# Kernel optimization log

Measured on AMD Instinct MI355X. Metric: run time of the kernel, lower is better.

Reference implementation:

```python
import jax, jax.numpy as jnp
import numpy as np

DEPTH = 2
TWO_PI = 6.283185307179586


def _apply_ry(state, theta, axis):
    """Apply RY(theta) on qubit at `axis` of state [N,2,2,2,2]. theta: [N] or scalar."""
    half = theta * 0.5
    a0 = jnp.take(state, 0, axis=axis)  # [N,2,2,2]
    a1 = jnp.take(state, 1, axis=axis)
    c = jnp.reshape(jnp.cos(half), (-1,) + (1,) * (a0.ndim - 1))
    s = jnp.reshape(jnp.sin(half), (-1,) + (1,) * (a0.ndim - 1))
    return jnp.stack([c * a0 - s * a1, s * a0 + c * a1], axis=axis)


def _apply_cnot(state, c_axis, t_axis):
    a0 = jnp.take(state, 0, axis=c_axis)  # control=0: unchanged
    a1 = jnp.take(state, 1, axis=c_axis)  # control=1: flip target
    t_ax = t_axis - (1 if t_axis > c_axis else 0)
    a1 = jnp.flip(a1, axis=t_ax)
    return jnp.stack([a0, a1], axis=c_axis)


def _simulate(patches, weights):
    """patches: [N,4] angles. Returns <Z_i> for i=0..3, shape [N,4]. All gates real."""
    N = patches.shape[0]
    state = jnp.zeros((N, 2, 2, 2, 2), dtype=patches.dtype)
    state = state.at[:, 0, 0, 0, 0].set(1.0)
    for w in range(4):  # data encoding
        state = _apply_ry(state, patches[:, w], axis=w + 1)
    for d in range(DEPTH):  # variational layers
        for w in range(4):
            state = _apply_ry(state, weights[d, w], axis=w + 1)
        for c, t in ((0, 1), (1, 2), (2, 3)):
            state = _apply_cnot(state, c + 1, t + 1)
    probs = state * state
    zs = []
    for w in range(4):
        p0 = jnp.take(probs, 0, axis=w + 1).sum(axis=(1, 2, 3))
        p1 = jnp.take(probs, 1, axis=w + 1).sum(axis=(1, 2, 3))
        zs.append(p0 - p1)
    return jnp.stack(zs, axis=-1)  # [N,4]


def setup_inputs() -> dict:
    key = jax.random.key(0)
    k1, k2, k3, k4 = jax.random.split(key, 4)
    B = 8192
    x = jax.random.uniform(k1, (B, 1, 28, 28), dtype=jnp.float32)
    weights = jax.random.uniform(k2, (DEPTH, 4), dtype=jnp.float32) * TWO_PI
    W = jax.random.normal(k3, (10, 4 * 14 * 14), dtype=jnp.float32) * 0.02
    b = jax.random.normal(k4, (10,), dtype=jnp.float32) * 0.02
    return {"x": x, "weights": weights, "W": W, "b": b}


def reference(x, weights, W, b):
    B = x.shape[0]
    # Extract non-overlapping 2x2 patches in row-major (i,j) order;
    # within a patch, order is [(i,j),(i,j+1),(i+1,j),(i+1,j+1)] matching x[:,:,i:i+2,j:j+2].view(B,4)
    p = x.reshape(B, 14, 2, 14, 2).transpose(0, 1, 3, 2, 4).reshape(B, 196, 4)
    feats = _simulate(p.reshape(B * 196, 4), weights).reshape(B, 196 * 4)
    logits = feats @ W.T + b
    return jax.nn.log_softmax(logits, axis=-1)
```

## Files before the change

### kernel.cpp

```cpp
#include <hip/hip_runtime.h>
#include <math.h>

#define INV2PI 0.15915494309189535f

__device__ __forceinline__ float rfl(float v) {
    return __int_as_float(__builtin_amdgcn_readfirstlane(__float_as_int(v)));
}

__global__ __launch_bounds__(256, 4) void quanv_ks_kernel(
    const float* __restrict__ x,
    const float* __restrict__ wts,
    const float* __restrict__ W,
    const float* __restrict__ bias,
    float* __restrict__ out,
    int B)
{
    __shared__ float part[4][8][40];
    __shared__ float logits[8][10];
    __shared__ float lsev[8];

    const int tid   = threadIdx.x;
    const int wave  = tid >> 6, lane = tid & 63;
    const int group = wave >> 1;
    const int half  = wave & 1;
    const int imgb  = blockIdx.x * 8 + group * 4;

    float w0r[4], cw1[4], sw1[4];
#pragma unroll
    for (int q = 0; q < 4; ++q) {
        w0r[q] = rfl(wts[q] * INV2PI);
        float r = wts[4 + q] * INV2PI;
        r -= floorf(r);
        cw1[q] = __builtin_amdgcn_cosf(r);
        sw1[q] = __builtin_amdgcn_sinf(r);
    }
    const float cc  = cw1[0]*cw1[1], cs = cw1[0]*sw1[1];
    const float sc  = sw1[0]*cw1[1], ss = sw1[0]*sw1[1];
    const float ccc = cc*cw1[2], ccs = cc*sw1[2], csc = cs*cw1[2], css = cs*sw1[2];
    const float scc = sc*cw1[2], ssc = ss*cw1[2], sss = ss*sw1[2];
    const float K0 = rfl(cw1[0]),       K1 = rfl(-sw1[0]);
    const float K2 = rfl(cc),           K3 = rfl(-cs),          K4 = rfl(ss);
    const float K5 = rfl(ccc),          K6 = rfl(-ccs),         K7 = rfl(css);
    const float K8 = rfl(-scc),         K9 = rfl(-sss);
    const float L1 = rfl(ccc*cw1[3]),   L2 = rfl(-ccc*sw1[3]);
    const float L3 = rfl(ccs*sw1[3]),   L4 = rfl(-csc*cw1[3]);
    const float L5 = rfl(-css*sw1[3]),  L6 = rfl(scc*sw1[3]);
    const float L7 = rfl(ssc*cw1[3]),   L8 = rfl(sss*sw1[3]);

    float acc[4][10];
#pragma unroll
    for (int im = 0; im < 4; ++im)
#pragma unroll
        for (int cl = 0; cl < 10; ++cl) acc[im][cl] = 0.f;

#pragma unroll
    for (int it = 0; it < 2; ++it) {
        if (it == 0 || lane < 34) {
            const int p  = half * 98 + it * 64 + lane;
            const int pi = p / 14, pj = p - pi * 14;
            const int xoff = pi * 56 + pj * 2;

            float z[4][4];
#pragma unroll
            for (int im = 0; im < 4; ++im) {
                const int img = imgb + im;
                if (img < B) {
                    const float* xp = x + (size_t)img * 784 + xoff;
                    const float2 t0 = *(const float2*)xp;
                    const float2 t1 = *(const float2*)(xp + 28);

                    float r;
                    r = fmaf(t0.x, INV2PI, w0r[0]); r -= floorf(r);
                    const float a  = __builtin_amdgcn_sinf(r), A  = __builtin_amdgcn_cosf(r);
                    r = fmaf(t0.y, INV2PI, w0r[1]); r -= floorf(r);
                    const float b  = __builtin_amdgcn_sinf(r), Bv = __builtin_amdgcn_cosf(r);
                    r = fmaf(t1.x, INV2PI, w0r[2]); r -= floorf(r);
                    const float c  = __builtin_amdgcn_sinf(r), C  = __builtin_amdgcn_cosf(r);
                    r = fmaf(t1.y, INV2PI, w0r[3]); r -= floorf(r);
                    const float d  = __builtin_amdgcn_sinf(r), D  = __builtin_amdgcn_cosf(r);

                    const float ab=a*b, bc=b*c, ac=a*c, cd=c*d, bd=b*d, ad=a*d;
                    const float AC=A*C, Ab=A*b, Bc=Bv*c, BD=Bv*D, cD=c*D, Cd=C*d;

                    z[im][0] = fmaf(K0, A,  K1*ab);
                    z[im][1] = fmaf(K2, Bv, fmaf(K3, A*bc, K4*ac));
                    z[im][2] = fmaf(K5, AC, fmaf(K6, Bv*cd,
                               fmaf(K7, A*bd, fmaf(K8, ab*C, K9*ad))));
                    z[im][3] = fmaf(L1, BD, fmaf(L2, AC*d, fmaf(L3, Bc,
                               fmaf(L4, Ab*cD, fmaf(L5, Ab, fmaf(L6, ab*Cd,
                               fmaf(L7, ac*D, L8*a)))))));
                } else {
                    z[im][0] = z[im][1] = z[im][2] = z[im][3] = 0.f;
                }
            }

#pragma unroll
            for (int cl = 0; cl < 10; ++cl) {
                const float4 wv = *(const float4*)(W + cl * 784 + p * 4);
#pragma unroll
                for (int im = 0; im < 4; ++im)
                    acc[im][cl] = fmaf(z[im][0], wv.x, fmaf(z[im][1], wv.y,
                                  fmaf(z[im][2], wv.z, fmaf(z[im][3], wv.w, acc[im][cl]))));
            }
        }
    }

#pragma unroll
    for (int im = 0; im < 4; ++im)
#pragma unroll
        for (int cl = 0; cl < 10; ++cl) {
            float v = acc[im][cl];
            v += __shfl_xor(v, 1, 64);
            v += __shfl_xor(v, 2, 64);
            v += __shfl_xor(v, 4, 64);
            if ((lane & 7) == 0) part[wave][lane >> 3][im * 10 + cl] = v;
        }
    __syncthreads();

    if (tid < 80) {
        const int g  = tid / 40;
        const int vv = tid - g * 40;
        const int im = vv / 10, cl = vv - im * 10;
        float s = 0.f;
#pragma unroll
        for (int l = 0; l < 8; ++l)
            s += part[2 * g][l][vv] + part[2 * g + 1][l][vv];
        logits[g * 4 + im][cl] = s + bias[cl];
    }
    __syncthreads();

    if (tid < 8) {
        if (blockIdx.x * 8 + tid < B) {
            float m = logits[tid][0];
#pragma unroll
            for (int cl = 1; cl < 10; ++cl) m = fmaxf(m, logits[tid][cl]);
            float s = 0.f;
#pragma unroll
            for (int cl = 0; cl < 10; ++cl) s += __expf(logits[tid][cl] - m);
            lsev[tid] = m + __logf(s);
        }
    }
    __syncthreads();

    if (tid < 80) {
        const int imloc = tid / 10, cl = tid - (tid / 10) * 10;
        const int img = blockIdx.x * 8 + imloc;
        if (img < B)
            out[(size_t)img * 10 + cl] = logits[imloc][cl] - lsev[imloc];
    }
}

extern "C" void kernel_launch(void* const* d_in, const int* in_sizes, int n_in,
                              void* d_out, int out_size, void* d_ws, size_t ws_size,
                              hipStream_t stream) {
    const float* x    = (const float*)d_in[0];
    const float* wts  = (const float*)d_in[1];
    const float* W    = (const float*)d_in[2];
    const float* bias = (const float*)d_in[3];
    float* out        = (float*)d_out;

    const int B = in_sizes[0] / 784;
    const int blocks = (B + 7) / 8;
    quanv_ks_kernel<<<blocks, 256, 0, stream>>>(x, wts, W, bias, out, B);
}
```

Before: 18.73 us.

## Process two adjacent patches per lane with float4 loads and hoisted input fetch

```diff
diff --git a/kernel.cpp b/kernel.cpp
--- a/kernel.cpp
+++ b/kernel.cpp
@@ -7,7 +7,7 @@
     return __int_as_float(__builtin_amdgcn_readfirstlane(__float_as_int(v)));
 }
 
-__global__ __launch_bounds__(256, 4) void quanv_ks_kernel(
+__global__ __launch_bounds__(256, 4) void quanv_r9_kernel(
     const float* __restrict__ x,
     const float* __restrict__ wts,
     const float* __restrict__ W,
@@ -25,14 +25,35 @@
     const int half  = wave & 1;
     const int imgb  = blockIdx.x * 8 + group * 4;
 
+    const bool act = (lane < 49);
+    const int q  = half * 49 + lane;
+    const int pi = q / 7;
+    const int pj = q - pi * 7;
+    const int xoff = pi * 56 + pj * 4;
+
+    float4 xt[4], xb[4];
+#pragma unroll
+    for (int im = 0; im < 4; ++im) {
+        xt[im] = make_float4(0.f, 0.f, 0.f, 0.f);
+        xb[im] = xt[im];
+    }
+    if (act) {
+#pragma unroll
+        for (int im = 0; im < 4; ++im) {
+            const float* xp = x + (size_t)(imgb + im) * 784 + xoff;
+            xt[im] = *(const float4*)xp;
+            xb[im] = *(const float4*)(xp + 28);
+        }
+    }
+
     float w0r[4], cw1[4], sw1[4];
 #pragma unroll
-    for (int q = 0; q < 4; ++q) {
-        w0r[q] = rfl(wts[q] * INV2PI);
-        float r = wts[4 + q] * INV2PI;
+    for (int qq = 0; qq < 4; ++qq) {
+        w0r[qq] = rfl(wts[qq] * INV2PI);
+        float r = wts[4 + qq] * INV2PI;
         r -= floorf(r);
-        cw1[q] = __builtin_amdgcn_cosf(r);
-        sw1[q] = __builtin_amdgcn_sinf(r);
+        cw1[qq] = __builtin_amdgcn_cosf(r);
+        sw1[qq] = __builtin_amdgcn_sinf(r);
     }
     const float cc  = cw1[0]*cw1[1], cs = cw1[0]*sw1[1];
     const float sc  = sw1[0]*cw1[1], ss = sw1[0]*sw1[1];
@@ -47,61 +68,59 @@
     const float L5 = rfl(-css*sw1[3]),  L6 = rfl(scc*sw1[3]);
     const float L7 = rfl(ssc*cw1[3]),   L8 = rfl(sss*sw1[3]);
 
+    float z[4][2][4];
+#pragma unroll
+    for (int im = 0; im < 4; ++im) {
+#pragma unroll
+        for (int h2 = 0; h2 < 2; ++h2) {
+            const float t0 = h2 ? xt[im].z : xt[im].x;
+            const float t1 = h2 ? xt[im].w : xt[im].y;
+            const float t2 = h2 ? xb[im].z : xb[im].x;
+            const float t3 = h2 ? xb[im].w : xb[im].y;
+
+            float r;
+            r = fmaf(t0, INV2PI, w0r[0]); r -= floorf(r);
+            const float a  = __builtin_amdgcn_sinf(r), A  = __builtin_amdgcn_cosf(r);
+            r = fmaf(t1, INV2PI, w0r[1]); r -= floorf(r);
+            const float b  = __builtin_amdgcn_sinf(r), Bv = __builtin_amdgcn_cosf(r);
+            r = fmaf(t2, INV2PI, w0r[2]); r -= floorf(r);
+            const float c  = __builtin_amdgcn_sinf(r), C  = __builtin_amdgcn_cosf(r);
+            r = fmaf(t3, INV2PI, w0r[3]); r -= floorf(r);
+            const float d  = __builtin_amdgcn_sinf(r), D  = __builtin_amdgcn_cosf(r);
+
+            const float ab=a*b, bc=b*c, ac=a*c, cd=c*d, bd=b*d, ad=a*d;
+            const float AC=A*C, Ab=A*b, Bc=Bv*c, BD=Bv*D, cD=c*D, Cd=C*d;
+
+            z[im][h2][0] = fmaf(K0, A,  K1*ab);
+            z[im][h2][1] = fmaf(K2, Bv, fmaf(K3, A*bc, K4*ac));
+            z[im][h2][2] = fmaf(K5, AC, fmaf(K6, Bv*cd,
+                           fmaf(K7, A*bd, fmaf(K8, ab*C, K9*ad))));
+            z[im][h2][3] = fmaf(L1, BD, fmaf(L2, AC*d, fmaf(L3, Bc,
+                           fmaf(L4, Ab*cD, fmaf(L5, Ab, fmaf(L6, ab*Cd,
+                           fmaf(L7, ac*D, L8*a)))))));
+        }
+    }
+
     float acc[4][10];
 #pragma unroll
     for (int im = 0; im < 4; ++im)
 #pragma unroll
         for (int cl = 0; cl < 10; ++cl) acc[im][cl] = 0.f;
 
+    if (act) {
+        const int kL = pi * 56 + pj * 8;
 #pragma unroll
-    for (int it = 0; it < 2; ++it) {
-        if (it == 0 || lane < 34) {
-            const int p  = half * 98 + it * 64 + lane;
-            const int pi = p / 14, pj = p - pi * 14;
-            const int xoff = pi * 56 + pj * 2;
-
-            float z[4][4];
+        for (int cl = 0; cl < 10; ++cl) {
+            const float* wp = W + cl * 784 + kL;
+            const float4 wvL = *(const float4*)wp;
+            const float4 wvR = *(const float4*)(wp + 4);
 #pragma unroll
-            for (int im = 0; im < 4; ++im) {
-                const int img = imgb + im;
-                if (img < B) {
-                    const float* xp = x + (size_t)img * 784 + xoff;
-                    const float2 t0 = *(const float2*)xp;
-                    const float2 t1 = *(const float2*)(xp + 28);
-
-                    float r;
-                    r = fmaf(t0.x, INV2PI, w0r[0]); r -= floorf(r);
-                    const float a  = __builtin_amdgcn_sinf(r), A  = __builtin_amdgcn_cosf(r);
-                    r = fmaf(t0.y, INV2PI, w0r[1]); r -= floorf(r);
-                    const float b  = __builtin_amdgcn_sinf(r), Bv = __builtin_amdgcn_cosf(r);
-                    r = fmaf(t1.x, INV2PI, w0r[2]); r -= floorf(r);
-                    const float c  = __builtin_amdgcn_sinf(r), C  = __builtin_amdgcn_cosf(r);
-                    r = fmaf(t1.y, INV2PI, w0r[3]); r -= floorf(r);
-                    const float d  = __builtin_amdgcn_sinf(r), D  = __builtin_amdgcn_cosf(r);
-
-                    const float ab=a*b, bc=b*c, ac=a*c, cd=c*d, bd=b*d, ad=a*d;
-                    const float AC=A*C, Ab=A*b, Bc=Bv*c, BD=Bv*D, cD=c*D, Cd=C*d;
-
-                    z[im][0] = fmaf(K0, A,  K1*ab);
-                    z[im][1] = fmaf(K2, Bv, fmaf(K3, A*bc, K4*ac));
-                    z[im][2] = fmaf(K5, AC, fmaf(K6, Bv*cd,
-                               fmaf(K7, A*bd, fmaf(K8, ab*C, K9*ad))));
-                    z[im][3] = fmaf(L1, BD, fmaf(L2, AC*d, fmaf(L3, Bc,
-                               fmaf(L4, Ab*cD, fmaf(L5, Ab, fmaf(L6, ab*Cd,
-                               fmaf(L7, ac*D, L8*a)))))));
-                } else {
-                    z[im][0] = z[im][1] = z[im][2] = z[im][3] = 0.f;
-                }
-            }
-
-#pragma unroll
-            for (int cl = 0; cl < 10; ++cl) {
-                const float4 wv = *(const float4*)(W + cl * 784 + p * 4);
-#pragma unroll
-                for (int im = 0; im < 4; ++im)
-                    acc[im][cl] = fmaf(z[im][0], wv.x, fmaf(z[im][1], wv.y,
-                                  fmaf(z[im][2], wv.z, fmaf(z[im][3], wv.w, acc[im][cl]))));
-            }
+            for (int im = 0; im < 4; ++im)
+                acc[im][cl] = fmaf(z[im][0][0], wvL.x, fmaf(z[im][0][1], wvL.y,
+                              fmaf(z[im][0][2], wvL.z, fmaf(z[im][0][3], wvL.w,
+                              fmaf(z[im][1][0], wvR.x, fmaf(z[im][1][1], wvR.y,
+                              fmaf(z[im][1][2], wvR.z, fmaf(z[im][1][3], wvR.w,
+                              acc[im][cl]))))))));
         }
     }
 
@@ -161,5 +180,5 @@
 
     const int B = in_sizes[0] / 784;
     const int blocks = (B + 7) / 8;
-    quanv_ks_kernel<<<blocks, 256, 0, stream>>>(x, wts, W, bias, out, B);
+    quanv_r9_kernel<<<blocks, 256, 0, stream>>>(x, wts, W, bias, out, B);
 }
```

New measurement: 17.82 us. 4.9% less time.
